# Performance work log

Hardware: AMD Instinct MI355X
Metric: run time of the kernel (lower is better)

The kernel has to match this reference:

```python
import jax, jax.numpy as jnp
import numpy as np

B, S, D = 4, 2048, 1024
INV_SCALE = 32.0  # sqrt(D)


def setup_inputs() -> dict:
    key = jax.random.key(0)
    ks = jax.random.split(key, 7)
    std = 1.0 / np.sqrt(D)
    return {
        "x1": jax.random.normal(ks[0], (B, S, D), dtype=jnp.float32),
        "Wq": jax.random.normal(ks[1], (D, D), dtype=jnp.float32) * std,
        "bq": jax.random.normal(ks[2], (D,), dtype=jnp.float32) * std,
        "Wk": jax.random.normal(ks[3], (D, D), dtype=jnp.float32) * std,
        "bk": jax.random.normal(ks[4], (D,), dtype=jnp.float32) * std,
        "Wv": jax.random.normal(ks[5], (D, D), dtype=jnp.float32) * std,
        "bv": jax.random.normal(ks[6], (D,), dtype=jnp.float32) * std,
    }


def reference(x1, Wq, bq, Wk, bk, Wv, bv):
    # Linear projections (torch Linear: y = x @ W^T + b)
    q = jnp.einsum("bsd,ed->bse", x1, Wq) + bq
    k = jnp.einsum("bsd,ed->bse", x1, Wk) + bk
    v = jnp.einsum("bsd,ed->bse", x1, Wv) + bv
    # Attention: QK^T / inv_scale -> softmax -> (dropout is identity in eval) -> @V
    scores = jnp.einsum("bqd,bkd->bqk", q, k) / INV_SCALE
    attn = jax.nn.softmax(scores, axis=-1)
    out = jnp.einsum("bqk,bkd->bqd", attn, v)
    return out
```

## Files before the change

### kernel.cpp

```cpp
#include <hip/hip_runtime.h>
#include <cstdint>
#include <cstddef>

using bf16 = __bf16;
typedef float f32x4 __attribute__((ext_vector_type(4)));
typedef __bf16 bf16x8v __attribute__((ext_vector_type(8)));
typedef __bf16 bf16x4v __attribute__((ext_vector_type(4)));

#define NX   8388608
#define NW   1048576
#define SB   2048
#define DD   1024

__device__ __forceinline__ void gload_lds16(const bf16* g, bf16* l) {
    __builtin_amdgcn_global_load_lds(
        (const __attribute__((address_space(1))) void*)(g),
        (__attribute__((address_space(3))) void*)(l), 16, 0, 0);
}

__global__ __launch_bounds__(256)
void convert_kernel(const float* __restrict__ x1,
                    const float* __restrict__ Wq, const float* __restrict__ Wk,
                    const float* __restrict__ Wv,
                    const float* __restrict__ bq, const float* __restrict__ bk,
                    const float* __restrict__ bv,
                    bf16* __restrict__ xb, bf16* __restrict__ wb,
                    float* __restrict__ biases)
{
    const int NX4 = NX / 4;
    const int NW4 = NW / 4;
    const int NMAT = NX4 + 3 * NW4;
    const int total = NMAT + 768;
    for (int i = blockIdx.x * 256 + threadIdx.x; i < total; i += gridDim.x * 256) {
        if (i < NMAT) {
            const float* src; bf16* dst; int j;
            if (i < NX4) { src = x1; dst = xb; j = i; }
            else {
                int w = (i - NX4) / NW4;
                j = (i - NX4) - w * NW4;
                src = (w == 0) ? Wq : (w == 1) ? Wk : Wv;
                dst = wb + (size_t)w * NW;
            }
            float4 f = ((const float4*)src)[j];
            bf16x4v o;
            o[0] = (bf16)f.x; o[1] = (bf16)f.y; o[2] = (bf16)f.z; o[3] = (bf16)f.w;
            ((bf16x4v*)dst)[j] = o;
        } else {
            int j = i - NMAT;
            const float* src = (j < 256) ? bq : (j < 512) ? bk : bv;
            ((float4*)biases)[j] = ((const float4*)src)[j & 255];
        }
    }
}

template<int V, typename OutT>
__global__ __launch_bounds__(256)
void gemm_bt(const bf16* __restrict__ A, const bf16* __restrict__ B,
             OutT* __restrict__ C, bf16* __restrict__ vT,
             const float* __restrict__ bias, float* __restrict__ pRow,
             int N, int K,
             long sAz, long sBz, long sCz, float scale)
{
    __shared__ bf16 lA[128 * 64];
    __shared__ bf16 lB[128 * 64];
    __shared__ float inv[128];
    const int z = blockIdx.z;
    A += (size_t)z * sAz;
    B += (size_t)z * sBz;
    C += (size_t)z * sCz;
    if constexpr (V == 1 || V == 2) pRow += (size_t)z * (SB * 32);

    const int gx = gridDim.x;
    const int nwg = gx * gridDim.y;
    const int orig = (int)blockIdx.y * gx + (int)blockIdx.x;
    const int q8 = nwg >> 3;
    const int tile = (orig & 7) * q8 + (orig >> 3);
    const int bx = tile % gx;
    const int by = tile / gx;

    const int n0 = bx * 128;
    const int m0 = by * 128;
    const int t = threadIdx.x;
    const int lane = t & 63;
    const int wid = t >> 6;
    const int wr = wid >> 1, wc = wid & 1;

    if constexpr (V == 2) {
        if (t < 128) {
            const float4* pr = (const float4*)&pRow[(size_t)(m0 + t) * 32];
            float s = 0.f;
            #pragma unroll
            for (int j = 0; j < 8; ++j) {
                float4 f = pr[j];
                s += f.x + f.y + f.z + f.w;
            }
            inv[t] = 1.0f / s;
        }
        __syncthreads();
    }

    f32x4 acc[4][4];
    #pragma unroll
    for (int m = 0; m < 4; ++m)
        #pragma unroll
        for (int n = 0; n < 4; ++n) acc[m][n] = (f32x4){0.f, 0.f, 0.f, 0.f};

    for (int k0 = 0; k0 < K; k0 += 64) {
        #pragma unroll
        for (int l = 0; l < 4; ++l) {
            const int idx = l * 256 + t;
            const int row = idx >> 3;
            const int c   = idx & 7;
            const int gc  = c ^ (row & 7);
            gload_lds16(A + (size_t)(m0 + row) * K + k0 + gc * 8, &lA[idx * 8]);
            gload_lds16(B + (size_t)(n0 + row) * K + k0 + gc * 8, &lB[idx * 8]);
        }
        __syncthreads();
        #pragma unroll
        for (int kk = 0; kk < 2; ++kk) {
            bf16x8v af[4], bfr[4];
            #pragma unroll
            for (int m = 0; m < 4; ++m) {
                const int row = wr * 64 + m * 16 + (lane & 15);
                const int ch  = (kk * 4 + (lane >> 4)) ^ (row & 7);
                af[m] = *(const bf16x8v*)&lA[row * 64 + ch * 8];
            }
            #pragma unroll
            for (int n = 0; n < 4; ++n) {
                const int row = wc * 64 + n * 16 + (lane & 15);
                const int ch  = (kk * 4 + (lane >> 4)) ^ (row & 7);
                bfr[n] = *(const bf16x8v*)&lB[row * 64 + ch * 8];
            }
            #pragma unroll
            for (int m = 0; m < 4; ++m)
                #pragma unroll
                for (int n = 0; n < 4; ++n)
                    acc[m][n] = __builtin_amdgcn_mfma_f32_16x16x32_bf16(
                        af[m], bfr[n], acc[m][n], 0, 0, 0);
        }
        __syncthreads();
    }

    const int cif = lane & 15;
    const int rif = (lane >> 4) << 2;

    if constexpr (V == 1) {
        float rs[4][4];
        #pragma unroll
        for (int m = 0; m < 4; ++m)
            #pragma unroll
            for (int r = 0; r < 4; ++r) rs[m][r] = 0.f;

        #pragma unroll
        for (int m = 0; m < 4; ++m) {
            const int gm = m0 + wr * 64 + m * 16 + rif;
            #pragma unroll
            for (int n = 0; n < 4; ++n) {
                const int col = n0 + wc * 64 + n * 16 + cif;
                #pragma unroll
                for (int r = 0; r < 4; ++r) {
                    const float e = __expf(acc[m][n][r] * scale - 6.0f);
                    rs[m][r] += e;
                    C[(size_t)(gm + r) * N + col] = (OutT)e;
                }
            }
        }
        #pragma unroll
        for (int m = 0; m < 4; ++m)
            #pragma unroll
            for (int r = 0; r < 4; ++r) {
                #pragma unroll
                for (int msk = 1; msk < 16; msk <<= 1)
                    rs[m][r] += __shfl_xor(rs[m][r], msk);
            }
        if ((lane & 15) == 0) {
            const int slot = bx * 2 + wc;
            #pragma unroll
            for (int m = 0; m < 4; ++m) {
                const int gm = m0 + wr * 64 + m * 16 + rif;
                #pragma unroll
                for (int r = 0; r < 4; ++r)
                    pRow[(size_t)(gm + r) * 32 + slot] = rs[m][r];
            }
        }
    } else {
        #pragma unroll
        for (int m = 0; m < 4; ++m) {
            const int gm = m0 + wr * 64 + m * 16 + rif;
            #pragma unroll
            for (int n = 0; n < 4; ++n) {
                const int col = n0 + wc * 64 + n * 16 + cif;
                if constexpr (V == 0) {
                    const float bb = bias[col];
                    if (col < 1024) {
                        #pragma unroll
                        for (int r = 0; r < 4; ++r)
                            C[(size_t)(gm + r) * 1024 + col] = (OutT)(acc[m][n][r] + bb);
                    } else if (col < 2048) {
                        #pragma unroll
                        for (int r = 0; r < 4; ++r)
                            C[NX + (size_t)(gm + r) * 1024 + (col - 1024)] = (OutT)(acc[m][n][r] + bb);
                    } else {
                        const int batch = gm >> 11, s = gm & 2047, d = col - 2048;
                        bf16x4v pk;
                        #pragma unroll
                        for (int r = 0; r < 4; ++r) pk[r] = (bf16)(acc[m][n][r] + bb);
                        *(bf16x4v*)&vT[((size_t)batch << 21) + ((size_t)d << 11) + s] = pk;
                    }
                } else {
                    const int rloc = wr * 64 + m * 16 + rif;
                    #pragma unroll
                    for (int r = 0; r < 4; ++r)
                        C[(size_t)(gm + r) * N + col] = (OutT)(acc[m][n][r] * inv[rloc + r]);
                }
            }
        }
    }
}

extern "C" void kernel_launch(void* const* d_in, const int* in_sizes, int n_in,
                              void* d_out, int out_size, void* d_ws, size_t ws_size,
                              hipStream_t stream)
{
    const float* x1 = (const float*)d_in[0];
    const float* Wq = (const float*)d_in[1];
    const float* bq = (const float*)d_in[2];
    const float* Wk = (const float*)d_in[3];
    const float* bk = (const float*)d_in[4];
    const float* Wv = (const float*)d_in[5];
    const float* bv = (const float*)d_in[6];
    float* out = (float*)d_out;

    bf16* xb     = (bf16*)d_ws;
    bf16* wb     = xb + NX;
    bf16* qkb    = wb + 3 * NW;
    bf16* vTb    = qkb + 2 * (size_t)NX;
    bf16* scores = vTb + NX;
    float* biases = (float*)(scores + 4 * (size_t)SB * SB);
    float* partial = (float*)xb;

    convert_kernel<<<dim3(2048), dim3(256), 0, stream>>>(
        x1, Wq, Wk, Wv, bq, bk, bv, xb, wb, biases);

    gemm_bt<0, bf16><<<dim3(24, 64, 1), dim3(256), 0, stream>>>(
        xb, wb, qkb, vTb, biases, nullptr, 1024, 1024, 0L, 0L, 0L, 1.0f);

    gemm_bt<1, bf16><<<dim3(16, 16, 4), dim3(256), 0, stream>>>(
        qkb, qkb + NX, scores, nullptr, nullptr, partial, SB, DD,
        (long)(SB * DD), (long)(SB * DD), (long)(SB * SB), 1.0f / 32.0f);

    gemm_bt<2, float><<<dim3(8, 16, 4), dim3(256), 0, stream>>>(
        scores, vTb, out, nullptr, nullptr, partial, DD, SB,
        (long)(SB * SB), (long)(SB * DD), (long)(SB * DD), 1.0f);
}
```

Measured before the change: 175.9 us.

## Use 256x256 eight-wave pipelined GEMM for QKV projection and QK^T

Adds a new 512-thread GEMM kernel with 256x256 output tiles, double-buffered LDS split into 128-row halves, and interleaved staging of the next K-slices between MFMA quadrants. Explicit vmcnt waits, barriers and setprio are used to overlap global-to-LDS loads with compute. It is applied to the QKV projection and the score GEMM, with exp2f/fma replacing expf in the softmax epilogue. The PV GEMM stays on the old 128x128 kernel, now specialised. The larger tiles raise data reuse but use more LDS and registers, lower occupancy, and give fewer workgroups per GEMM.

New measurement: 177.8 us. About the same (+1.0%).

```diff
diff --git a/kernel.cpp b/kernel.cpp
--- a/kernel.cpp
+++ b/kernel.cpp
@@ -11,6 +11,8 @@
 #define NW   1048576
 #define SB   2048
 #define DD   1024
+
+#define VMCNT(n) asm volatile("s_waitcnt vmcnt(" #n ")" ::: "memory")
 
 __device__ __forceinline__ void gload_lds16(const bf16* g, bf16* l) {
     __builtin_amdgcn_global_load_lds(
@@ -54,12 +56,193 @@
 }
 
 template<int V, typename OutT>
+__global__ __launch_bounds__(512)
+void gemm8(const bf16* __restrict__ A, const bf16* __restrict__ B,
+           OutT* __restrict__ C, bf16* __restrict__ vT,
+           const float* __restrict__ bias, float* __restrict__ pRow,
+           int N, int K, int NXT, long sA, long sB, long sC, float scale)
+{
+    __shared__ bf16 shA[2][2][8192];
+    __shared__ bf16 shB[2][2][8192];
+    const int z = blockIdx.z;
+    A += (size_t)z * sA; B += (size_t)z * sB; C += (size_t)z * sC;
+    if constexpr (V == 1) pRow += (size_t)z * (SB * 32);
+
+    const int nwg = gridDim.x;
+    const int q8 = nwg >> 3;
+    const int tile = ((int)blockIdx.x & 7) * q8 + ((int)blockIdx.x >> 3);
+    const int bx = tile % NXT, by = tile / NXT;
+    const int n0 = bx * 256, m0 = by * 256;
+
+    const int tid = threadIdx.x;
+    const int lane = tid & 63, wid = tid >> 6;
+    const int wr = wid >> 2, wc = wid & 3;
+    const int rl = lane & 15, lg = lane >> 4;
+    const int wr16 = wr * 16, wc16 = wc * 16;
+
+    const bf16* Ag = A + (size_t)m0 * K;
+    const bf16* Bg = B + (size_t)n0 * K;
+
+    auto stg = [&](const bf16* g, bf16* l) {
+        #pragma unroll
+        for (int j = 0; j < 2; ++j) {
+            const int idx = j * 512 + tid;
+            const int row = idx >> 3;
+            const int c = idx & 7;
+            gload_lds16(g + (size_t)row * K + ((c ^ (row & 7)) << 3), l + idx * 8);
+        }
+    };
+
+    f32x4 acc[8][4];
+    #pragma unroll
+    for (int m = 0; m < 8; ++m)
+        #pragma unroll
+        for (int n = 0; n < 4; ++n) acc[m][n] = (f32x4){0.f, 0.f, 0.f, 0.f};
+
+    const int NT = K >> 6;
+
+    stg(Ag, &shA[0][0][0]);
+    stg(Bg, &shB[0][0][0]);
+    stg(Ag + (size_t)128 * K, &shA[0][1][0]);
+    stg(Bg + (size_t)128 * K, &shB[0][1][0]);
+    stg(Ag + 64, &shA[1][0][0]);
+    stg(Bg + 64, &shB[1][0][0]);
+    VMCNT(4);
+    __builtin_amdgcn_s_barrier();
+
+    bf16x8v af[4][2], bfr[2][2];
+
+#define RD_A(mq)                                                               \
+    {                                                                          \
+        const bf16* ap = &shA[buf][mq][0];                                     \
+        _Pragma("unroll") for (int i = 0; i < 4; ++i)                          \
+            _Pragma("unroll") for (int kk = 0; kk < 2; ++kk) {                 \
+                const int r = i * 32 + wr16 + rl;                              \
+                af[i][kk] = *(const bf16x8v*)&ap[r * 64 +                      \
+                    (((kk * 4 + lg) ^ (r & 7)) << 3)];                         \
+            }                                                                  \
+    }
+#define RD_B(nq)                                                               \
+    {                                                                          \
+        const bf16* bp = &shB[buf][nq][0];                                     \
+        _Pragma("unroll") for (int n = 0; n < 2; ++n)                          \
+            _Pragma("unroll") for (int kk = 0; kk < 2; ++kk) {                 \
+                const int r = n * 64 + wc16 + rl;                              \
+                bfr[n][kk] = *(const bf16x8v*)&bp[r * 64 +                     \
+                    (((kk * 4 + lg) ^ (r & 7)) << 3)];                         \
+            }                                                                  \
+    }
+#define MM(mq, nq)                                                             \
+    __builtin_amdgcn_s_barrier();                                              \
+    asm volatile("s_waitcnt lgkmcnt(0)" ::: "memory");                         \
+    __builtin_amdgcn_sched_barrier(0);                                         \
+    __builtin_amdgcn_s_setprio(1);                                             \
+    _Pragma("unroll") for (int i = 0; i < 4; ++i)                              \
+        _Pragma("unroll") for (int n = 0; n < 2; ++n)                          \
+            _Pragma("unroll") for (int kk = 0; kk < 2; ++kk)                   \
+                acc[mq * 4 + i][nq * 2 + n] =                                  \
+                    __builtin_amdgcn_mfma_f32_16x16x32_bf16(                   \
+                        af[i][kk], bfr[n][kk], acc[mq * 4 + i][nq * 2 + n],    \
+                        0, 0, 0);                                              \
+    __builtin_amdgcn_s_setprio(0);                                             \
+    __builtin_amdgcn_s_barrier();
+
+    for (int t = 0; t < NT; ++t) {
+        const int buf = t & 1;
+        RD_A(0); RD_B(0);
+        if (t + 1 < NT) stg(Ag + (size_t)128 * K + (t + 1) * 64, &shA[buf ^ 1][1][0]);
+        MM(0, 0);
+        RD_A(1);
+        if (t + 1 < NT) stg(Bg + (size_t)128 * K + (t + 1) * 64, &shB[buf ^ 1][1][0]);
+        MM(1, 0);
+        RD_A(0); RD_B(1);
+        if (t + 2 < NT) stg(Bg + (t + 2) * 64, &shB[buf][0][0]);
+        MM(0, 1);
+        RD_A(1);
+        if (t + 2 < NT) stg(Ag + (t + 2) * 64, &shA[buf][0][0]);
+        if (t + 2 >= NT) { VMCNT(0); } else { VMCNT(4); }
+        MM(1, 1);
+    }
+#undef RD_A
+#undef RD_B
+#undef MM
+
+    const int cif = rl;
+    const int rif = lg << 2;
+
+    if constexpr (V == 1) {
+        const float sc2 = scale * 1.4426950408889634f;
+        const float sh2 = -8.656170245333781f;
+        float rs[8][4];
+        #pragma unroll
+        for (int m = 0; m < 8; ++m)
+            #pragma unroll
+            for (int r = 0; r < 4; ++r) rs[m][r] = 0.f;
+
+        #pragma unroll
+        for (int m = 0; m < 8; ++m) {
+            const int grow = m0 + m * 32 + wr16 + rif;
+            #pragma unroll
+            for (int n = 0; n < 4; ++n) {
+                const int col = n0 + n * 64 + wc16 + cif;
+                #pragma unroll
+                for (int r = 0; r < 4; ++r) {
+                    const float e = exp2f(fmaf(acc[m][n][r], sc2, sh2));
+                    rs[m][r] += e;
+                    C[(size_t)(grow + r) * N + col] = (OutT)e;
+                }
+            }
+        }
+        #pragma unroll
+        for (int m = 0; m < 8; ++m)
+            #pragma unroll
+            for (int r = 0; r < 4; ++r) {
+                #pragma unroll
+                for (int msk = 1; msk < 16; msk <<= 1)
+                    rs[m][r] += __shfl_xor(rs[m][r], msk);
+            }
+        if (rl == 0) {
+            const int slot = bx * 4 + wc;
+            #pragma unroll
+            for (int m = 0; m < 8; ++m) {
+                const int grow = m0 + m * 32 + wr16 + rif;
+                #pragma unroll
+                for (int r = 0; r < 4; ++r)
+                    pRow[(size_t)(grow + r) * 32 + slot] = rs[m][r];
+            }
+        }
+    } else {
+        #pragma unroll
+        for (int m = 0; m < 8; ++m) {
+            const int grow = m0 + m * 32 + wr16 + rif;
+            #pragma unroll
+            for (int n = 0; n < 4; ++n) {
+                const int col = n0 + n * 64 + wc16 + cif;
+                const float bb = bias[col];
+                if (col < 1024) {
+                    #pragma unroll
+                    for (int r = 0; r < 4; ++r)
+                        C[(size_t)(grow + r) * 1024 + col] = (OutT)(acc[m][n][r] + bb);
+                } else if (col < 2048) {
+                    #pragma unroll
+                    for (int r = 0; r < 4; ++r)
+                        C[NX + (size_t)(grow + r) * 1024 + (col - 1024)] = (OutT)(acc[m][n][r] + bb);
+                } else {
+                    const int batch = grow >> 11, s = grow & 2047, d = col - 2048;
+                    bf16x4v pk;
+                    #pragma unroll
+                    for (int r = 0; r < 4; ++r) pk[r] = (bf16)(acc[m][n][r] + bb);
+                    *(bf16x4v*)&vT[((size_t)batch << 21) + ((size_t)d << 11) + s] = pk;
+                }
+            }
+        }
+    }
+}
+
 __global__ __launch_bounds__(256)
-void gemm_bt(const bf16* __restrict__ A, const bf16* __restrict__ B,
-             OutT* __restrict__ C, bf16* __restrict__ vT,
-             const float* __restrict__ bias, float* __restrict__ pRow,
-             int N, int K,
-             long sAz, long sBz, long sCz, float scale)
+void gemm_pv(const bf16* __restrict__ A, const bf16* __restrict__ B,
+             float* __restrict__ C, const float* __restrict__ pRow,
+             int N, int K, long sAz, long sBz, long sCz)
 {
     __shared__ bf16 lA[128 * 64];
     __shared__ bf16 lB[128 * 64];
@@ -68,7 +251,7 @@
     A += (size_t)z * sAz;
     B += (size_t)z * sBz;
     C += (size_t)z * sCz;
-    if constexpr (V == 1 || V == 2) pRow += (size_t)z * (SB * 32);
+    pRow += (size_t)z * (SB * 32);
 
     const int gx = gridDim.x;
     const int nwg = gx * gridDim.y;
@@ -85,19 +268,17 @@
     const int wid = t >> 6;
     const int wr = wid >> 1, wc = wid & 1;
 
-    if constexpr (V == 2) {
-        if (t < 128) {
-            const float4* pr = (const float4*)&pRow[(size_t)(m0 + t) * 32];
-            float s = 0.f;
-            #pragma unroll
-            for (int j = 0; j < 8; ++j) {
-                float4 f = pr[j];
-                s += f.x + f.y + f.z + f.w;
-            }
-            inv[t] = 1.0f / s;
-        }
-        __syncthreads();
-    }
+    if (t < 128) {
+        const float4* pr = (const float4*)&pRow[(size_t)(m0 + t) * 32];
+        float s = 0.f;
+        #pragma unroll
+        for (int j = 0; j < 8; ++j) {
+            float4 f = pr[j];
+            s += f.x + f.y + f.z + f.w;
+        }
+        inv[t] = 1.0f / s;
+    }
+    __syncthreads();
 
     f32x4 acc[4][4];
     #pragma unroll
@@ -143,77 +324,16 @@
 
     const int cif = lane & 15;
     const int rif = (lane >> 4) << 2;
-
-    if constexpr (V == 1) {
-        float rs[4][4];
-        #pragma unroll
-        for (int m = 0; m < 4; ++m)
-            #pragma unroll
-            for (int r = 0; r < 4; ++r) rs[m][r] = 0.f;
-
-        #pragma unroll
-        for (int m = 0; m < 4; ++m) {
-            const int gm = m0 + wr * 64 + m * 16 + rif;
-            #pragma unroll
-            for (int n = 0; n < 4; ++n) {
-                const int col = n0 + wc * 64 + n * 16 + cif;
-                #pragma unroll
-                for (int r = 0; r < 4; ++r) {
-                    const float e = __expf(acc[m][n][r] * scale - 6.0f);
-                    rs[m][r] += e;
-                    C[(size_t)(gm + r) * N + col] = (OutT)e;
-                }
-            }
-        }
-        #pragma unroll
-        for (int m = 0; m < 4; ++m)
-            #pragma unroll
-            for (int r = 0; r < 4; ++r) {
-                #pragma unroll
-                for (int msk = 1; msk < 16; msk <<= 1)
-                    rs[m][r] += __shfl_xor(rs[m][r], msk);
-            }
-        if ((lane & 15) == 0) {
-            const int slot = bx * 2 + wc;
-            #pragma unroll
-            for (int m = 0; m < 4; ++m) {
-                const int gm = m0 + wr * 64 + m * 16 + rif;
-                #pragma unroll
-                for (int r = 0; r < 4; ++r)
-                    pRow[(size_t)(gm + r) * 32 + slot] = rs[m][r];
-            }
-        }
-    } else {
-        #pragma unroll
-        for (int m = 0; m < 4; ++m) {
-            const int gm = m0 + wr * 64 + m * 16 + rif;
-            #pragma unroll
-            for (int n = 0; n < 4; ++n) {
-                const int col = n0 + wc * 64 + n * 16 + cif;
-                if constexpr (V == 0) {
-                    const float bb = bias[col];
-                    if (col < 1024) {
-                        #pragma unroll
-                        for (int r = 0; r < 4; ++r)
-                            C[(size_t)(gm + r) * 1024 + col] = (OutT)(acc[m][n][r] + bb);
-                    } else if (col < 2048) {
-                        #pragma unroll
-                        for (int r = 0; r < 4; ++r)
-                            C[NX + (size_t)(gm + r) * 1024 + (col - 1024)] = (OutT)(acc[m][n][r] + bb);
-                    } else {
-                        const int batch = gm >> 11, s = gm & 2047, d = col - 2048;
-                        bf16x4v pk;
-                        #pragma unroll
-                        for (int r = 0; r < 4; ++r) pk[r] = (bf16)(acc[m][n][r] + bb);
-                        *(bf16x4v*)&vT[((size_t)batch << 21) + ((size_t)d << 11) + s] = pk;
-                    }
-                } else {
-                    const int rloc = wr * 64 + m * 16 + rif;
-                    #pragma unroll
-                    for (int r = 0; r < 4; ++r)
-                        C[(size_t)(gm + r) * N + col] = (OutT)(acc[m][n][r] * inv[rloc + r]);
-                }
-            }
+    #pragma unroll
+    for (int m = 0; m < 4; ++m) {
+        const int gm = m0 + wr * 64 + m * 16 + rif;
+        const int rloc = wr * 64 + m * 16 + rif;
+        #pragma unroll
+        for (int n = 0; n < 4; ++n) {
+            const int col = n0 + wc * 64 + n * 16 + cif;
+            #pragma unroll
+            for (int r = 0; r < 4; ++r)
+                C[(size_t)(gm + r) * N + col] = acc[m][n][r] * inv[rloc + r];
         }
     }
 }
@@ -242,14 +362,14 @@
     convert_kernel<<<dim3(2048), dim3(256), 0, stream>>>(
         x1, Wq, Wk, Wv, bq, bk, bv, xb, wb, biases);
 
-    gemm_bt<0, bf16><<<dim3(24, 64, 1), dim3(256), 0, stream>>>(
-        xb, wb, qkb, vTb, biases, nullptr, 1024, 1024, 0L, 0L, 0L, 1.0f);
-
-    gemm_bt<1, bf16><<<dim3(16, 16, 4), dim3(256), 0, stream>>>(
-        qkb, qkb + NX, scores, nullptr, nullptr, partial, SB, DD,
+    gemm8<0, bf16><<<dim3(384, 1, 1), dim3(512), 0, stream>>>(
+        xb, wb, qkb, vTb, biases, nullptr, 1024, 1024, 12, 0L, 0L, 0L, 1.0f);
+
+    gemm8<1, bf16><<<dim3(64, 1, 4), dim3(512), 0, stream>>>(
+        qkb, qkb + NX, scores, nullptr, nullptr, partial, SB, DD, 8,
         (long)(SB * DD), (long)(SB * DD), (long)(SB * SB), 1.0f / 32.0f);
 
-    gemm_bt<2, float><<<dim3(8, 16, 4), dim3(256), 0, stream>>>(
-        scores, vTb, out, nullptr, nullptr, partial, DD, SB,
-        (long)(SB * SB), (long)(SB * DD), (long)(SB * DD), 1.0f);
-}
+    gemm_pv<<<dim3(8, 16, 4), dim3(256), 0, stream>>>(
+        scores, vTb, out, partial, DD, SB,
+        (long)(SB * SB), (long)(SB * DD), (long)(SB * DD));
+}
```

## Double-buffer LDS tiles in GEMM to overlap global loads with MFMA

Applied to the files above, without the earlier changes.

Splits each shared-memory tile into two buffers and prefetches the tile two steps ahead with global_load_lds, using explicit vmcnt waits and barriers. All fragments are read into registers before the next load is issued into the same buffer, so global memory latency is meant to overlap the MFMA work. The softmax-exp epilogue also switches to exp2 with a fused multiply-add. Doubling the LDS footprint to about 64KB may lower occupancy, and the hand-written waitcnt counts must match the number of loads issued per stage.

After: 162.3 us. 1.08x faster.

```diff
diff --git a/kernel.cpp b/kernel.cpp
--- a/kernel.cpp
+++ b/kernel.cpp
@@ -61,8 +61,8 @@
              int N, int K,
              long sAz, long sBz, long sCz, float scale)
 {
-    __shared__ bf16 lA[128 * 64];
-    __shared__ bf16 lB[128 * 64];
+    __shared__ bf16 lA[2][128 * 64];
+    __shared__ bf16 lB[2][128 * 64];
     __shared__ float inv[128];
     const int z = blockIdx.z;
     A += (size_t)z * sAz;
@@ -105,46 +105,67 @@
         #pragma unroll
         for (int n = 0; n < 4; ++n) acc[m][n] = (f32x4){0.f, 0.f, 0.f, 0.f};
 
-    for (int k0 = 0; k0 < K; k0 += 64) {
+    auto stage = [&](int b, int k0) {
         #pragma unroll
         for (int l = 0; l < 4; ++l) {
             const int idx = l * 256 + t;
             const int row = idx >> 3;
             const int c   = idx & 7;
             const int gc  = c ^ (row & 7);
-            gload_lds16(A + (size_t)(m0 + row) * K + k0 + gc * 8, &lA[idx * 8]);
-            gload_lds16(B + (size_t)(n0 + row) * K + k0 + gc * 8, &lB[idx * 8]);
-        }
-        __syncthreads();
+            gload_lds16(A + (size_t)(m0 + row) * K + k0 + gc * 8, &lA[b][idx * 8]);
+            gload_lds16(B + (size_t)(n0 + row) * K + k0 + gc * 8, &lB[b][idx * 8]);
+        }
+    };
+
+    const int NT = K >> 6;
+
+    stage(0, 0);
+    stage(1, 64);
+
+    for (int tt = 0; tt < NT; ++tt) {
+        const int cur = tt & 1;
+        if (tt == NT - 1) asm volatile("s_waitcnt vmcnt(0)" ::: "memory");
+        else              asm volatile("s_waitcnt vmcnt(8)" ::: "memory");
+        __builtin_amdgcn_s_barrier();
+
+        bf16x8v af[2][4], bfr[2][4];
         #pragma unroll
         for (int kk = 0; kk < 2; ++kk) {
-            bf16x8v af[4], bfr[4];
             #pragma unroll
             for (int m = 0; m < 4; ++m) {
                 const int row = wr * 64 + m * 16 + (lane & 15);
                 const int ch  = (kk * 4 + (lane >> 4)) ^ (row & 7);
-                af[m] = *(const bf16x8v*)&lA[row * 64 + ch * 8];
+                af[kk][m] = *(const bf16x8v*)&lA[cur][row * 64 + ch * 8];
             }
             #pragma unroll
             for (int n = 0; n < 4; ++n) {
                 const int row = wc * 64 + n * 16 + (lane & 15);
                 const int ch  = (kk * 4 + (lane >> 4)) ^ (row & 7);
-                bfr[n] = *(const bf16x8v*)&lB[row * 64 + ch * 8];
-            }
+                bfr[kk][n] = *(const bf16x8v*)&lB[cur][row * 64 + ch * 8];
+            }
+        }
+        asm volatile("s_waitcnt lgkmcnt(0)" ::: "memory");
+        __builtin_amdgcn_sched_barrier(0);
+        __builtin_amdgcn_s_barrier();
+
+        if (tt + 2 < NT) stage(cur, (tt + 2) * 64);
+
+        #pragma unroll
+        for (int kk = 0; kk < 2; ++kk)
             #pragma unroll
             for (int m = 0; m < 4; ++m)
                 #pragma unroll
                 for (int n = 0; n < 4; ++n)
                     acc[m][n] = __builtin_amdgcn_mfma_f32_16x16x32_bf16(
-                        af[m], bfr[n], acc[m][n], 0, 0, 0);
-        }
-        __syncthreads();
+                        af[kk][m], bfr[kk][n], acc[m][n], 0, 0, 0);
     }
 
     const int cif = lane & 15;
     const int rif = (lane >> 4) << 2;
 
     if constexpr (V == 1) {
+        const float sc2 = scale * 1.4426950408889634f;
+        const float sh2 = -8.656170245333781f;
         float rs[4][4];
         #pragma unroll
         for (int m = 0; m < 4; ++m)
@@ -159,7 +180,7 @@
                 const int col = n0 + wc * 64 + n * 16 + cif;
                 #pragma unroll
                 for (int r = 0; r < 4; ++r) {
-                    const float e = __expf(acc[m][n][r] * scale - 6.0f);
+                    const float e = exp2f(fmaf(acc[m][n][r], sc2, sh2));
                     rs[m][r] += e;
                     C[(size_t)(gm + r) * N + col] = (OutT)e;
                 }
```
